# Kernel tuning notes

Measured on AMD Instinct MI355X. Metric: run time of the kernel, lower is better.

The kernel has to match this reference:

```python
import jax, jax.numpy as jnp
import numpy as np

B, C, H, W, N = 16, 80, 100, 100, 32
LAMBDA_L1, LAMBDA_GIOU, POS_IOU_THR = 1.0, 2.0, 0.3
# pos_radius=1.5 with python int() truncation on non-negative max_i/max_j gives
# window rows/cols in [idx-2, idx+1] clipped to the grid (verified vs torch code).
R_LO, R_HI = 2, 1


def _make_boxes(key, shape):
    kc, ks = jax.random.split(key)
    c = jax.random.uniform(kc, shape + (2,), minval=0.1, maxval=0.9)
    s = jax.random.uniform(ks, shape + (2,), minval=0.05, maxval=0.3)
    return jnp.concatenate([c - s * 0.5, c + s * 0.5], axis=-1)  # valid xyxy


def setup_inputs() -> dict:
    key = jax.random.key(0)
    k1, k2, k3 = jax.random.split(key, 3)
    pred_boxes = _make_boxes(k1, (B, C, H, W))        # [B,C,H,W,4]
    gt_boxes = _make_boxes(k2, (B, N))                # [B,N,4]
    gt_labels = jax.random.randint(k3, (B, N), 0, C)  # [B,N] in [0,C)
    return {"pred_boxes": pred_boxes, "gt_boxes": gt_boxes, "gt_labels": gt_labels}


def giou_fn(a, b):
    # a: [...,4], b broadcastable [...,4], xyxy. Same math as torchvision generalized_box_iou.
    area_a = (a[..., 2] - a[..., 0]) * (a[..., 3] - a[..., 1])
    area_b = (b[..., 2] - b[..., 0]) * (b[..., 3] - b[..., 1])
    lt = jnp.maximum(a[..., :2], b[..., :2])
    rb = jnp.minimum(a[..., 2:], b[..., 2:])
    wh = jnp.clip(rb - lt, 0.0)
    inter = wh[..., 0] * wh[..., 1]
    union = area_a + area_b - inter
    iou = inter / union
    lt_c = jnp.minimum(a[..., :2], b[..., :2])
    rb_c = jnp.maximum(a[..., 2:], b[..., 2:])
    wh_c = jnp.clip(rb_c - lt_c, 0.0)
    area_c = wh_c[..., 0] * wh_c[..., 1]
    return iou - (area_c - union) / area_c


def reference(pred_boxes, gt_boxes, gt_labels):
    _, _, h, w, _ = pred_boxes.shape
    rows = jnp.arange(h)
    cols = jnp.arange(w)

    def per_gt(pred_img, gt_box, label):
        # pred_img: [C,H,W,4], gt_box: [4], label: scalar int
        grid = pred_img[label]                      # [H,W,4] gather over class dim
        g = giou_fn(grid, gt_box)                   # [H,W] GIoU vs this GT
        flat = g.reshape(-1)
        idx = jnp.argmax(flat)                      # row-major, matches torch argmax on [H,W]
        max_iou = flat[idx]
        mi, mj = idx // w, idx % w
        rmask = (rows >= mi - R_LO) & (rows <= jnp.minimum(mi + R_HI, h - 1))
        cmask = (cols >= mj - R_LO) & (cols <= jnp.minimum(mj + R_HI, w - 1))
        mask = (rmask[:, None] & cmask[None, :]).astype(grid.dtype)  # [H,W] window
        valid = (max_iou > POS_IOU_THR).astype(grid.dtype)
        l1 = jnp.abs(grid - gt_box).mean(-1)        # F.l1_loss per cell (mean over 4 coords)
        return (valid * jnp.sum(l1 * mask),
                valid * jnp.sum((1.0 - g) * mask),
                valid * jnp.sum(mask))

    per_img = jax.vmap(per_gt, in_axes=(None, 0, 0))   # over N GTs
    l1s, gious, cnts = jax.vmap(per_img)(pred_boxes, gt_boxes, gt_labels)  # over B
    n_pos = jnp.sum(cnts)
    denom = jnp.maximum(n_pos, 1.0)
    loss_l1 = jnp.sum(l1s) / denom
    loss_giou = jnp.sum(gious) / denom
    loss_total = LAMBDA_L1 * loss_l1 + LAMBDA_GIOU * loss_giou
    return loss_total
```

## Files before the change

kernel.cpp:

```cpp
#include <hip/hip_runtime.h>

constexpr int B_ = 16, C_ = 80, H_ = 100, W_ = 100, N_ = 32;
constexpr int HW = H_ * W_;
constexpr int BN = B_ * N_;
constexpr float POS_THR = 0.3f;
constexpr int TPB = 1024;

__device__ __forceinline__ float rcpf(float x) { return __builtin_amdgcn_rcpf(x); }

__device__ __forceinline__ float giou4(const float4 a,
                                       const float gx0, const float gy0,
                                       const float gx1, const float gy1,
                                       const float area_b) {
    float area_a = (a.z - a.x) * (a.w - a.y);
    float ltx = fmaxf(a.x, gx0), lty = fmaxf(a.y, gy0);
    float rbx = fminf(a.z, gx1), rby = fminf(a.w, gy1);
    float iw = fmaxf(rbx - ltx, 0.0f), ih = fmaxf(rby - lty, 0.0f);
    float inter = iw * ih;
    float uni = area_a + area_b - inter;
    float cx0 = fminf(a.x, gx0), cy0 = fminf(a.y, gy0);
    float cx1 = fmaxf(a.z, gx1), cy1 = fmaxf(a.w, gy1);
    float area_c = (cx1 - cx0) * (cy1 - cy0);
    return inter * rcpf(uni) + uni * rcpf(area_c) - 1.0f;
}

__global__ __launch_bounds__(TPB, 8) void per_gt_kernel(
    const float* __restrict__ pred,
    const float* __restrict__ gt,
    const int*   __restrict__ labels,
    float* __restrict__ ws)
{
    const int bn = blockIdx.x;
    const int b  = bn / N_;
    const int label = labels[bn];
    const float4 g4 = reinterpret_cast<const float4*>(gt)[bn];
    const float area_b = (g4.z - g4.x) * (g4.w - g4.y);
    const float4* __restrict__ base =
        reinterpret_cast<const float4*>(pred) + ((size_t)b * C_ + label) * HW;

    float best = -3.0f;
    int   bi   = HW;
    int i = threadIdx.x;
    for (; i + TPB < HW; i += 2 * TPB) {
        float4 a0 = base[i];
        float4 a1 = base[i + TPB];
        float g0 = giou4(a0, g4.x, g4.y, g4.z, g4.w, area_b);
        float g1 = giou4(a1, g4.x, g4.y, g4.z, g4.w, area_b);
        if (g0 > best) { best = g0; bi = i; }
        if (g1 > best) { best = g1; bi = i + TPB; }
    }
    if (i < HW) {
        float g = giou4(base[i], g4.x, g4.y, g4.z, g4.w, area_b);
        if (g > best) { best = g; bi = i; }
    }

    #pragma unroll
    for (int off = 32; off; off >>= 1) {
        float ov = __shfl_down(best, off, 64);
        int   oi = __shfl_down(bi,   off, 64);
        if (ov > best || (ov == best && oi < bi)) { best = ov; bi = oi; }
    }

    __shared__ float sv[16];
    __shared__ int   si[16];
    const int wid  = threadIdx.x >> 6;
    const int lane = threadIdx.x & 63;
    if (lane == 0) { sv[wid] = best; si[wid] = bi; }
    __syncthreads();

    if (wid != 0) return;

    best = (lane < 16) ? sv[lane] : -3.0f;
    bi   = (lane < 16) ? si[lane] : HW;
    #pragma unroll
    for (int off = 8; off; off >>= 1) {
        float ov = __shfl_down(best, off, 16);
        int   oi = __shfl_down(bi,   off, 16);
        if (ov > best || (ov == best && oi < bi)) { best = ov; bi = oi; }
    }
    best = __shfl(best, 0, 64);
    bi   = __shfl(bi,   0, 64);

    float sl1 = 0.0f, sg = 0.0f, ct = 0.0f;
    if (best > POS_THR) {
        const int mi = bi / W_, mj = bi % W_;
        const int r0 = max(mi - 2, 0), r1 = min(mi + 1, H_ - 1);
        const int c0 = max(mj - 2, 0), c1 = min(mj + 1, W_ - 1);
        const int r = r0 + (lane >> 2);
        const int c = c0 + (lane & 3);
        if (lane < 16 && r <= r1 && c <= c1) {
            float4 a = base[r * W_ + c];
            float g = giou4(a, g4.x, g4.y, g4.z, g4.w, area_b);
            sl1 = 0.25f * (fabsf(a.x - g4.x) + fabsf(a.y - g4.y) +
                           fabsf(a.z - g4.z) + fabsf(a.w - g4.w));
            sg = 1.0f - g;
            ct = 1.0f;
        }
        #pragma unroll
        for (int off = 8; off; off >>= 1) {
            sl1 += __shfl_down(sl1, off, 16);
            sg  += __shfl_down(sg,  off, 16);
            ct  += __shfl_down(ct,  off, 16);
        }
    }
    if (lane == 0) {
        ws[bn]          = sl1;
        ws[BN + bn]     = sg;
        ws[2 * BN + bn] = ct;
    }
}

__global__ __launch_bounds__(BN) void finalize_kernel(
    const float* __restrict__ ws, float* __restrict__ out)
{
    const int t = threadIdx.x;
    float l1 = ws[t], gi = ws[BN + t], ct = ws[2 * BN + t];
    #pragma unroll
    for (int off = 32; off; off >>= 1) {
        l1 += __shfl_down(l1, off, 64);
        gi += __shfl_down(gi, off, 64);
        ct += __shfl_down(ct, off, 64);
    }
    __shared__ float s0[8], s1[8], s2[8];
    const int wid = t >> 6;
    if ((t & 63) == 0) { s0[wid] = l1; s1[wid] = gi; s2[wid] = ct; }
    __syncthreads();
    if (t == 0) {
        float L = 0.0f, G = 0.0f, Cn = 0.0f;
        #pragma unroll
        for (int w = 0; w < BN / 64; ++w) { L += s0[w]; G += s1[w]; Cn += s2[w]; }
        const float denom = fmaxf(Cn, 1.0f);
        out[0] = L / denom + 2.0f * (G / denom);
    }
}

extern "C" void kernel_launch(void* const* d_in, const int* in_sizes, int n_in,
                              void* d_out, int out_size, void* d_ws, size_t ws_size,
                              hipStream_t stream) {
    const float* pred   = (const float*)d_in[0];
    const float* gt     = (const float*)d_in[1];
    const int*   labels = (const int*)d_in[2];
    float* ws  = (float*)d_ws;
    float* out = (float*)d_out;

    per_gt_kernel<<<BN, TPB, 0, stream>>>(pred, gt, labels, ws);
    finalize_kernel<<<1, BN, 0, stream>>>(ws, out);
}
```

Baseline: 22.16 us.

## Fuse finalize into main kernel via atomic ticket and spin-waiting extra block

```diff
diff --git a/kernel.cpp b/kernel.cpp
--- a/kernel.cpp
+++ b/kernel.cpp
@@ -24,13 +24,50 @@
     return inter * rcpf(uni) + uni * rcpf(area_c) - 1.0f;
 }
 
-__global__ __launch_bounds__(TPB, 8) void per_gt_kernel(
+__global__ __launch_bounds__(TPB, 8) void fused_kernel(
     const float* __restrict__ pred,
     const float* __restrict__ gt,
     const int*   __restrict__ labels,
-    float* __restrict__ ws)
+    float* __restrict__ ws,
+    float* __restrict__ out)
 {
-    const int bn = blockIdx.x;
+    const int blk  = blockIdx.x;
+    const int lane = threadIdx.x & 63;
+    const int wid  = threadIdx.x >> 6;
+
+    if (blk == BN) {
+        if (threadIdx.x == 0) {
+            unsigned* ticket = (unsigned*)(ws + 3 * BN);
+            while (atomicAdd(ticket, 0u) < (unsigned)BN)
+                __builtin_amdgcn_s_sleep(8);
+        }
+        __syncthreads();
+        float l1 = 0.0f, gi = 0.0f, cn = 0.0f;
+        if (threadIdx.x < BN) {
+            l1 = atomicAdd(&ws[threadIdx.x], 0.0f);
+            gi = atomicAdd(&ws[BN + threadIdx.x], 0.0f);
+            cn = atomicAdd(&ws[2 * BN + threadIdx.x], 0.0f);
+        }
+        #pragma unroll
+        for (int off = 32; off; off >>= 1) {
+            l1 += __shfl_down(l1, off, 64);
+            gi += __shfl_down(gi, off, 64);
+            cn += __shfl_down(cn, off, 64);
+        }
+        __shared__ float s0[16], s1[16], s2[16];
+        if (lane == 0) { s0[wid] = l1; s1[wid] = gi; s2[wid] = cn; }
+        __syncthreads();
+        if (threadIdx.x == 0) {
+            float L = 0.0f, G = 0.0f, Cn = 0.0f;
+            #pragma unroll
+            for (int w = 0; w < 16; ++w) { L += s0[w]; G += s1[w]; Cn += s2[w]; }
+            const float denom = fmaxf(Cn, 1.0f);
+            out[0] = L / denom + 2.0f * (G / denom);
+        }
+        return;
+    }
+
+    const int bn = blk;
     const int b  = bn / N_;
     const int label = labels[bn];
     const float4 g4 = reinterpret_cast<const float4*>(gt)[bn];
@@ -63,8 +100,6 @@
 
     __shared__ float sv[16];
     __shared__ int   si[16];
-    const int wid  = threadIdx.x >> 6;
-    const int lane = threadIdx.x & 63;
     if (lane == 0) { sv[wid] = best; si[wid] = bi; }
     __syncthreads();
 
@@ -104,33 +139,11 @@
         }
     }
     if (lane == 0) {
-        ws[bn]          = sl1;
-        ws[BN + bn]     = sg;
-        ws[2 * BN + bn] = ct;
-    }
-}
-
-__global__ __launch_bounds__(BN) void finalize_kernel(
-    const float* __restrict__ ws, float* __restrict__ out)
-{
-    const int t = threadIdx.x;
-    float l1 = ws[t], gi = ws[BN + t], ct = ws[2 * BN + t];
-    #pragma unroll
-    for (int off = 32; off; off >>= 1) {
-        l1 += __shfl_down(l1, off, 64);
-        gi += __shfl_down(gi, off, 64);
-        ct += __shfl_down(ct, off, 64);
-    }
-    __shared__ float s0[8], s1[8], s2[8];
-    const int wid = t >> 6;
-    if ((t & 63) == 0) { s0[wid] = l1; s1[wid] = gi; s2[wid] = ct; }
-    __syncthreads();
-    if (t == 0) {
-        float L = 0.0f, G = 0.0f, Cn = 0.0f;
-        #pragma unroll
-        for (int w = 0; w < BN / 64; ++w) { L += s0[w]; G += s1[w]; Cn += s2[w]; }
-        const float denom = fmaxf(Cn, 1.0f);
-        out[0] = L / denom + 2.0f * (G / denom);
+        atomicExch(&ws[bn], sl1);
+        atomicExch(&ws[BN + bn], sg);
+        atomicExch(&ws[2 * BN + bn], ct);
+        asm volatile("s_waitcnt vmcnt(0)" ::: "memory");
+        atomicAdd((unsigned*)(ws + 3 * BN), 1u);
     }
 }
 
@@ -143,6 +156,6 @@
     float* ws  = (float*)d_ws;
     float* out = (float*)d_out;
 
-    per_gt_kernel<<<BN, TPB, 0, stream>>>(pred, gt, labels, ws);
-    finalize_kernel<<<1, BN, 0, stream>>>(ws, out);
+    hipMemsetAsync(ws + 3 * BN, 0, sizeof(unsigned), stream);
+    fused_kernel<<<BN + 1, TPB, 0, stream>>>(pred, gt, labels, ws, out);
 }
```

Result: slower. 29.69 us (+34.0%).
